# Kernel optimization log

Measured on AMD Instinct MI355X. Metric: run time of the kernel, lower is better.

The kernel has to match this reference:

```python
import jax, jax.numpy as jnp
import numpy as np

N = 8192        # points
M = 131072      # query-key pairs (edges)
C_IN = 512
H = 8           # heads
D = 64          # head_channels
BINS = 48
BIN_SIZE = 0.05


def setup_inputs() -> dict:
    key = jax.random.key(0)
    ks = jax.random.split(key, 8)
    x_F = jax.random.normal(ks[0], (N, C_IN), dtype=jnp.float32)
    x_C = jax.random.uniform(ks[1], (N, 3), dtype=jnp.float32)
    qk_pair_idxs = jax.random.randint(ks[2], (2, M), 0, N, dtype=jnp.int64)
    W_qkv = jax.random.normal(ks[3], (C_IN, 3 * H * D), dtype=jnp.float32) * 0.02
    b_qkv = jnp.zeros((3 * H * D,), dtype=jnp.float32)
    q_tables = jax.random.normal(ks[4], (3, BINS, H, D), dtype=jnp.float32) * 0.02
    k_tables = jax.random.normal(ks[5], (3, BINS, H, D), dtype=jnp.float32) * 0.02
    v_tables = jax.random.normal(ks[6], (3, BINS, H, D), dtype=jnp.float32) * 0.02
    return {"x_F": x_F, "x_C": x_C, "qk_pair_idxs": qk_pair_idxs,
            "W_qkv": W_qkv, "b_qkv": b_qkv,
            "q_tables": q_tables, "k_tables": k_tables, "v_tables": v_tables}


def reference(x_F, x_C, qk_pair_idxs, W_qkv, b_qkv, q_tables, k_tables, v_tables):
    n = x_F.shape[0]
    qkv = (x_F @ W_qkv + b_qkv).reshape(n, 3, H, D)
    q = qkv[:, 0] * (D ** -0.5)   # scale folded into queries, as in the module
    k = qkv[:, 1]
    v = qkv[:, 2]
    qi = qk_pair_idxs[0]
    ki = qk_pair_idxs[1]
    # quantized relative coordinates -> table bin indices [M,3]
    rel = (x_C[qi] - x_C[ki]) / BIN_SIZE + BINS / 2
    idx = jnp.clip(rel.astype(jnp.int32), 0, BINS - 1)
    # precompute per-point, per-axis, per-bin table dot products [N,3,BINS,H]
    q_dot = jnp.einsum('nhd,abhd->nabh', q, q_tables)
    k_dot = jnp.einsum('nhd,abhd->nabh', k, k_tables)
    # content logits [M,H]
    logits = jnp.einsum('mhd,mhd->mh', q[qi], k[ki])
    for a in range(3):  # fixed xyz axes
        logits = logits + q_dot[qi, a, idx[:, a]] + k_dot[ki, a, idx[:, a]]
    # scatter softmax over query index (per head)
    seg_max = jax.ops.segment_max(logits, qi, num_segments=n)
    e = jnp.exp(logits - seg_max[qi])
    denom = jax.ops.segment_sum(e, qi, num_segments=n)
    attn = e / denom[qi]  # [M,H]
    # value-side relative position bias, summed over axes [M,H,D]
    vt = v_tables[0, idx[:, 0]] + v_tables[1, idx[:, 1]] + v_tables[2, idx[:, 2]]
    contrib = attn[:, :, None] * (v[ki] + vt)            # [M,H,D]
    agg = jax.ops.segment_sum(contrib, qi, num_segments=n)  # [N,H,D]
    return agg.reshape(n, H * D)
```

## Files before the change

### kernel.cpp

```cpp
#include <hip/hip_runtime.h>
#include <hip/hip_bf16.h>
#include <stdint.h>

#define N_PTS 8192
#define M_EDGES 131072
#define CIN 512
#define QKV_COLS 1536

typedef __bf16 bf16x8 __attribute__((ext_vector_type(8)));
typedef float f32x4 __attribute__((ext_vector_type(4)));

#define GAS __attribute__((address_space(1)))
#define LAS __attribute__((address_space(3)))

__device__ __forceinline__ void gload_lds16(const void* g, void* l) {
  __builtin_amdgcn_global_load_lds((const GAS void*)g, (LAS void*)l, 16, 0, 0);
}

__global__ __launch_bounds__(256) void prep_kernel(
    const float* __restrict__ xF, const float* __restrict__ W,
    const float* __restrict__ qt, const float* __restrict__ kt,
    const float* __restrict__ vt, const int* __restrict__ pairs,
    const float* __restrict__ xc,
    __bf16* __restrict__ A, __bf16* __restrict__ BT,
    __bf16* __restrict__ qtb, __bf16* __restrict__ ktb, __bf16* __restrict__ vtT,
    int* __restrict__ qi_a, unsigned* __restrict__ pack0, int* __restrict__ cnt) {
  __shared__ float tile[32][33];
  int b = blockIdx.x;
  int tid = threadIdx.x;
  if (b < 4096) {
    int base = (b * 256 + tid) * 4;
    float4 v = *(const float4*)(xF + base);
    A[base + 0] = (__bf16)v.x;
    A[base + 1] = (__bf16)v.y;
    A[base + 2] = (__bf16)v.z;
    A[base + 3] = (__bf16)v.w;
  } else if (b < 4864) {
    int blk = b - 4096;
    int bk = blk & 15, bn = blk >> 4;
    int x = tid & 31, y = tid >> 5;
#pragma unroll
    for (int j = 0; j < 4; j++) {
      int r = y + j * 8;
      tile[r][x] = W[(size_t)(bk * 32 + r) * QKV_COLS + bn * 32 + x];
    }
    __syncthreads();
#pragma unroll
    for (int j = 0; j < 4; j++) {
      int r = y + j * 8;
      BT[(size_t)(bn * 32 + r) * CIN + bk * 32 + x] = (__bf16)tile[x][r];
    }
  } else if (b < 5152) {
    int i = (b - 4864) * 256 + tid;
    int d = i & 63, h = (i >> 6) & 7, ab = i >> 9;
    int po = (h * 144 + ab) * 64 + d;
    qtb[po] = (__bf16)qt[i];
    ktb[po] = (__bf16)kt[i];
  } else if (b < 5472) {
    int i = (b - 5152) * 256 + tid;
    int p = i % 160;
    int d = (i / 160) & 63;
    int h = i / 10240;
    vtT[i] = (p < 144) ? (__bf16)vt[p * 512 + h * 64 + d] : (__bf16)0.f;
  } else {
    int m = (b - 5472) * 256 + tid;
    int qi = pairs[m], ki = pairs[M_EDGES + m];
    unsigned pb = 0;
#pragma unroll
    for (int a = 0; a < 3; a++) {
      float rel = (xc[qi * 3 + a] - xc[ki * 3 + a]) / 0.05f + 24.0f;
      int bb = (int)rel;
      bb = bb < 0 ? 0 : (bb > 47 ? 47 : bb);
      pb |= (unsigned)bb << (6 * a);
    }
    qi_a[m] = qi;
    pack0[m] = (unsigned)ki | (pb << 13);
    atomicAdd(&cnt[qi], 1);
  }
}

__global__ __launch_bounds__(256) void gemm_qkv(const __bf16* __restrict__ A,
                                                const __bf16* __restrict__ BT,
                                                const float* __restrict__ bias,
                                                __bf16* __restrict__ qb,
                                                __bf16* __restrict__ kb,
                                                __bf16* __restrict__ vb) {
  __shared__ __align__(16) char At[64 * 128];
  __shared__ __align__(16) char Bt[128 * 128];
  int tid = threadIdx.x;
  int w = tid >> 6, l = tid & 63;
  int bm = blockIdx.x, bn = blockIdx.y;
  int wm = w & 1, wn = w >> 1;
  f32x4 acc[2][4] = {};
  const char* Ab = (const char*)A;
  const char* Bb = (const char*)BT;
  int lr = l & 15;
  int lk = (l >> 4) * 16;
  int xr = (lr & 7) << 4;

  for (int kt = 0; kt < 8; kt++) {
#pragma unroll
    for (int r = 0; r < 2; r++) {
      int flat = r * 4096 + tid * 16;
      int row = flat >> 7, colb = flat & 127;
      int gcolb = colb ^ ((row & 7) << 4);
      gload_lds16(Ab + ((size_t)(bm * 64 + row) * CIN + kt * 64) * 2 + gcolb,
                  At + r * 4096 + w * 1024);
    }
#pragma unroll
    for (int r = 0; r < 4; r++) {
      int flat = r * 4096 + tid * 16;
      int row = flat >> 7, colb = flat & 127;
      int gcolb = colb ^ ((row & 7) << 4);
      gload_lds16(Bb + ((size_t)(bn * 128 + row) * CIN + kt * 64) * 2 + gcolb,
                  Bt + r * 4096 + w * 1024);
    }
    __syncthreads();
#pragma unroll
    for (int ks = 0; ks < 2; ks++) {
      bf16x8 af[2], bfr[4];
      int cs = (ks * 64 + lk) ^ xr;
#pragma unroll
      for (int mf = 0; mf < 2; mf++) af[mf] = *(const bf16x8*)(At + (wm * 32 + mf * 16 + lr) * 128 + cs);
#pragma unroll
      for (int nf = 0; nf < 4; nf++) bfr[nf] = *(const bf16x8*)(Bt + (wn * 64 + nf * 16 + lr) * 128 + cs);
#pragma unroll
      for (int mf = 0; mf < 2; mf++)
#pragma unroll
        for (int nf = 0; nf < 4; nf++)
          acc[mf][nf] = __builtin_amdgcn_mfma_f32_16x16x32_bf16(af[mf], bfr[nf], acc[mf][nf], 0, 0, 0);
    }
    __syncthreads();
  }

  int lg = l >> 4;
#pragma unroll
  for (int mf = 0; mf < 2; mf++) {
#pragma unroll
    for (int nf = 0; nf < 4; nf++) {
      int gc = bn * 128 + wn * 64 + nf * 16 + lr;
      float b = bias[gc];
      int which = gc >> 9;
      int col = gc & 511;
      __bf16* dst = which == 0 ? qb : (which == 1 ? kb : vb);
      float scale = which == 0 ? 0.125f : 1.0f;
#pragma unroll
      for (int j = 0; j < 4; j++) {
        int gr = bm * 64 + wm * 32 + mf * 16 + lg * 4 + j;
        dst[(size_t)gr * 512 + col] = (__bf16)((acc[mf][nf][j] + b) * scale);
      }
    }
  }
}

__global__ __launch_bounds__(256) void table_dot(const __bf16* __restrict__ qb,
                                                 const __bf16* __restrict__ kb,
                                                 const __bf16* __restrict__ qtb,
                                                 const __bf16* __restrict__ ktb,
                                                 __bf16* __restrict__ qdot,
                                                 __bf16* __restrict__ kdot) {
  __shared__ __align__(16) char As[128 * 128];
  __shared__ __align__(16) char Bs[144 * 128];
  int nt = blockIdx.x, h = blockIdx.y, z = blockIdx.z;
  const __bf16* src = z ? kb : qb;
  const __bf16* tab = z ? ktb : qtb;
  __bf16* out = z ? kdot : qdot;
  int tid = threadIdx.x, w = tid >> 6, l = tid & 63;
  const char* sb = (const char*)src;
  const char* tb = (const char*)tab + (size_t)h * 144 * 128;
#pragma unroll
  for (int p = 0; p < 4; p++) {
    int flat = p * 4096 + tid * 16;
    int row = flat >> 7, colb = flat & 127;
    int gcolb = colb ^ ((row & 7) << 4);
    gload_lds16(sb + (size_t)(nt * 128 + row) * 1024 + h * 128 + gcolb, As + p * 4096 + w * 1024);
    gload_lds16(tb + row * 128 + gcolb, Bs + p * 4096 + w * 1024);
  }
  if (w < 2) {
    int flat = 16384 + w * 1024 + l * 16;
    int row = flat >> 7, colb = flat & 127;
    int gcolb = colb ^ ((row & 7) << 4);
    gload_lds16(tb + row * 128 + gcolb, Bs + 16384 + w * 1024);
  }
  __syncthreads();

  f32x4 acc[2][9] = {};
  int lr = l & 15, lk = (l >> 4) * 16;
  int xr = (lr & 7) << 4;
#pragma unroll
  for (int ks = 0; ks < 2; ks++) {
    bf16x8 af[2], bf[9];
    int cs = (ks * 64 + lk) ^ xr;
#pragma unroll
    for (int mf = 0; mf < 2; mf++)
      af[mf] = *(const bf16x8*)(As + (w * 32 + mf * 16 + lr) * 128 + cs);
#pragma unroll
    for (int nf = 0; nf < 9; nf++)
      bf[nf] = *(const bf16x8*)(Bs + (nf * 16 + lr) * 128 + cs);
#pragma unroll
    for (int mf = 0; mf < 2; mf++)
#pragma unroll
      for (int nf = 0; nf < 9; nf++)
        acc[mf][nf] = __builtin_amdgcn_mfma_f32_16x16x32_bf16(af[mf], bf[nf], acc[mf][nf], 0, 0, 0);
  }

  int lg = l >> 4;
#pragma unroll
  for (int mf = 0; mf < 2; mf++)
#pragma unroll
    for (int nf = 0; nf < 9; nf++)
#pragma unroll
      for (int j = 0; j < 4; j++) {
        int n = nt * 128 + w * 32 + mf * 16 + lg * 4 + j;
        int ab = nf * 16 + lr;
        out[(size_t)n * 1152 + ab * 8 + h] = (__bf16)acc[mf][nf][j];
      }
}

__global__ __launch_bounds__(256) void scan_kernel(const int* __restrict__ cnt,
                                                   int* __restrict__ off,
                                                   int* __restrict__ cursor) {
  __shared__ int wsum[4];
  int tid = threadIdx.x, lane = tid & 63, w = tid >> 6;
  int local[32];
  int s = 0;
#pragma unroll
  for (int i = 0; i < 8; i++) {
    int4 v = ((const int4*)cnt)[tid * 8 + i];
    local[i * 4 + 0] = v.x; local[i * 4 + 1] = v.y;
    local[i * 4 + 2] = v.z; local[i * 4 + 3] = v.w;
    s += v.x + v.y + v.z + v.w;
  }
  int incl = s;
#pragma unroll
  for (int d = 1; d < 64; d <<= 1) {
    int t = __shfl_up(incl, d, 64);
    if (lane >= d) incl += t;
  }
  if (lane == 63) wsum[w] = incl;
  __syncthreads();
  int woff = 0;
#pragma unroll
  for (int j = 0; j < 4; j++) woff += (j < w) ? wsum[j] : 0;
  int run = woff + incl - s;
  int base = tid * 32;
#pragma unroll
  for (int i = 0; i < 32; i++) {
    off[base + i] = run;
    cursor[base + i] = run;
    run += local[i];
  }
  if (tid == 255) off[N_PTS] = run;
}

__global__ void scatter_k(const int* __restrict__ qi_a, const unsigned* __restrict__ pack0,
                          int* __restrict__ cursor, int* __restrict__ qi_s,
                          unsigned* __restrict__ epack) {
  int m = blockIdx.x * blockDim.x + threadIdx.x;
  if (m < M_EDGES) {
    int qi = qi_a[m];
    int pos = atomicAdd(&cursor[qi], 1);
    qi_s[pos] = qi;
    epack[pos] = pack0[m];
  }
}

__global__ void edge_bias(const int* __restrict__ qi_s, const unsigned* __restrict__ epack,
                          const __bf16* __restrict__ qdot, const __bf16* __restrict__ kdot,
                          float* __restrict__ eb) {
  int t = blockIdx.x * 256 + threadIdx.x;
  int e = t >> 3, h = t & 7;
  unsigned pk = epack[e];
  int ki = pk & 8191;
  unsigned pb = pk >> 13;
  int qi = qi_s[e];
  int a0 = ((int)(pb & 63)) * 8 + h;
  int a1 = (48 + (int)((pb >> 6) & 63)) * 8 + h;
  int a2 = (96 + (int)((pb >> 12) & 63)) * 8 + h;
  const __bf16* qd = qdot + qi * 1152;
  const __bf16* kd = kdot + ki * 1152;
  eb[t] = (float)qd[a0] + (float)qd[a1] + (float)qd[a2] +
          (float)kd[a0] + (float)kd[a1] + (float)kd[a2];
}

__global__ __launch_bounds__(512) void attn_kernel(
    const __bf16* __restrict__ qb, const __bf16* __restrict__ kb,
    const __bf16* __restrict__ vb, const float* __restrict__ eb,
    const int* __restrict__ off, const unsigned* __restrict__ epack,
    float* __restrict__ num, float* __restrict__ den, __bf16* __restrict__ Hb) {
  __shared__ float hist[8 * 160];
  int n = blockIdx.x;
  int tid = threadIdx.x;
  int h = tid >> 6, l = tid & 63;
  int es = l >> 3, dg = l & 7;
  int tcol = h * 64 + dg * 8;

  for (int i = tid; i < 1280; i += 512) hist[i] = 0.f;
  __syncthreads();

  bf16x8 q8 = *(const bf16x8*)(qb + (n << 9) + tcol);
  float qv[8];
#pragma unroll
  for (int j = 0; j < 8; j++) qv[j] = (float)q8[j];

  float acc[8] = {0.f, 0.f, 0.f, 0.f, 0.f, 0.f, 0.f, 0.f};
  float dn = 0.f;
  int e0 = off[n], e1 = off[n + 1];

  for (int base = e0; base < e1; base += 8) {
    int e = base + es;
    bool valid = e < e1;
    int ee = valid ? e : e0;
    unsigned pk = epack[ee];
    float ebv = eb[(ee << 3) + h];
    int ki = pk & 8191;
    unsigned pb = pk >> 13;
    bf16x8 k8 = *(const bf16x8*)(kb + (ki << 9) + tcol);
    bf16x8 v8 = *(const bf16x8*)(vb + (ki << 9) + tcol);
    float p = 0.f;
#pragma unroll
    for (int j = 0; j < 8; j++) p += qv[j] * (float)k8[j];
    p += __shfl_xor(p, 1, 64);
    p += __shfl_xor(p, 2, 64);
    p += __shfl_xor(p, 4, 64);
    p += ebv;
    float x = valid ? __expf(p) : 0.f;
    dn += x;
#pragma unroll
    for (int j = 0; j < 8; j++) acc[j] += x * (float)v8[j];
    if (dg == 0 && valid) {
      float* hh = hist + h * 160;
      atomicAdd(hh + (pb & 63), x);
      atomicAdd(hh + 48 + ((pb >> 6) & 63), x);
      atomicAdd(hh + 96 + ((pb >> 12) & 63), x);
    }
  }

#pragma unroll
  for (int s = 8; s <= 32; s <<= 1) {
    dn += __shfl_xor(dn, s, 64);
#pragma unroll
    for (int j = 0; j < 8; j++) acc[j] += __shfl_xor(acc[j], s, 64);
  }

  if (l < 8) {
    float* op = num + (n << 9) + h * 64 + l * 8;
    f32x4 o0 = {acc[0], acc[1], acc[2], acc[3]};
    f32x4 o1 = {acc[4], acc[5], acc[6], acc[7]};
    *(f32x4*)op = o0;
    *(f32x4*)(op + 4) = o1;
  }
  if (l == 0) den[n * 8 + h] = dn;
  __syncthreads();
  for (int i = tid; i < 1280; i += 512) Hb[(size_t)n * 1280 + i] = (__bf16)hist[i];
}

__global__ __launch_bounds__(256) void finish_kernel(const __bf16* __restrict__ Hb,
                                                     const __bf16* __restrict__ vtT,
                                                     const float* __restrict__ den,
                                                     float* __restrict__ out) {
  __shared__ __align__(16) char As[128 * 64];
  __shared__ __align__(16) char Bs[64 * 64];
  int nt = blockIdx.x, h = blockIdx.y;
  int tid = threadIdx.x, w = tid >> 6, l = tid & 63;
  int lr = l & 15, lk = (l >> 4) * 16;
  int xr = (lr & 3) << 4;
  const char* Ab = (const char*)Hb;
  const char* Bb = (const char*)vtT;
  f32x4 acc[2][4] = {};

  for (int kt = 0; kt < 5; kt++) {
#pragma unroll
    for (int c = 0; c < 2; c++) {
      int flat = c * 4096 + tid * 16;
      int row = flat >> 6, colb = flat & 63;
      int gcolb = colb ^ ((row & 3) << 4);
      gload_lds16(Ab + ((size_t)(nt * 128 + row) * 1280 + h * 160 + kt * 32) * 2 + gcolb,
                  As + c * 4096 + w * 1024);
    }
    {
      int flat = tid * 16;
      int row = flat >> 6, colb = flat & 63;
      int gcolb = colb ^ ((row & 3) << 4);
      gload_lds16(Bb + ((size_t)(h * 64 + row) * 160 + kt * 32) * 2 + gcolb,
                  Bs + w * 1024);
    }
    __syncthreads();
    bf16x8 af[2], bf[4];
    int cs = lk ^ xr;
#pragma unroll
    for (int mf = 0; mf < 2; mf++) af[mf] = *(const bf16x8*)(As + (w * 32 + mf * 16 + lr) * 64 + cs);
#pragma unroll
    for (int nf = 0; nf < 4; nf++) bf[nf] = *(const bf16x8*)(Bs + (nf * 16 + lr) * 64 + cs);
#pragma unroll
    for (int mf = 0; mf < 2; mf++)
#pragma unroll
      for (int nf = 0; nf < 4; nf++)
        acc[mf][nf] = __builtin_amdgcn_mfma_f32_16x16x32_bf16(af[mf], bf[nf], acc[mf][nf], 0, 0, 0);
    __syncthreads();
  }

  int lg = l >> 4;
#pragma unroll
  for (int mf = 0; mf < 2; mf++) {
#pragma unroll
    for (int j = 0; j < 4; j++) {
      int n = nt * 128 + w * 32 + mf * 16 + lg * 4 + j;
      float dnv = den[n * 8 + h];
      float inv = dnv > 0.f ? 1.f / dnv : 0.f;
#pragma unroll
      for (int nf = 0; nf < 4; nf++) {
        int gi = (n << 9) + h * 64 + nf * 16 + lr;
        out[gi] = (out[gi] + acc[mf][nf][j]) * inv;
      }
    }
  }
}

extern "C" void kernel_launch(void* const* d_in, const int* in_sizes, int n_in,
                              void* d_out, int out_size, void* d_ws, size_t ws_size,
                              hipStream_t stream) {
  const float* xF = (const float*)d_in[0];
  const float* xC = (const float*)d_in[1];
  const int* pairs = (const int*)d_in[2];
  const float* W = (const float*)d_in[3];
  const float* bias = (const float*)d_in[4];
  const float* qt = (const float*)d_in[5];
  const float* kt = (const float*)d_in[6];
  const float* vt = (const float*)d_in[7];
  float* out = (float*)d_out;

  char* ws = (char*)d_ws;
  size_t o = 0;
  auto alloc = [&](size_t bytes) {
    void* p = ws + o;
    o = (o + bytes + 255) & ~(size_t)255;
    return p;
  };
  char* region0 = (char*)alloc((size_t)N_PTS * 1280 * 2);
  __bf16* A = (__bf16*)region0;
  __bf16* BT = (__bf16*)(region0 + (size_t)N_PTS * CIN * 2);
  __bf16* Hb = (__bf16*)region0;
  __bf16* qb = (__bf16*)alloc((size_t)N_PTS * 512 * 2);
  __bf16* kb = (__bf16*)alloc((size_t)N_PTS * 512 * 2);
  __bf16* vb = (__bf16*)alloc((size_t)N_PTS * 512 * 2);
  __bf16* qtb = (__bf16*)alloc((size_t)8 * 144 * 64 * 2);
  __bf16* ktb = (__bf16*)alloc((size_t)8 * 144 * 64 * 2);
  __bf16* vtT = (__bf16*)alloc((size_t)8 * 64 * 160 * 2);
  __bf16* qdot = (__bf16*)alloc((size_t)N_PTS * 1152 * 2);
  __bf16* kdot = (__bf16*)alloc((size_t)N_PTS * 1152 * 2);
  float* eb = (float*)alloc((size_t)M_EDGES * 8 * 4);
  float* den = (float*)alloc((size_t)N_PTS * 8 * 4);
  int* qi_a = (int*)alloc(M_EDGES * 4);
  unsigned* pack0 = (unsigned*)alloc(M_EDGES * 4);
  int* qi_s = (int*)alloc(M_EDGES * 4);
  unsigned* epack = (unsigned*)alloc(M_EDGES * 4);
  int* cnt = (int*)alloc(N_PTS * 4);
  int* off = (int*)alloc((N_PTS + 1) * 4);
  int* cursor = (int*)alloc(N_PTS * 4);

  hipMemsetAsync(cnt, 0, N_PTS * 4, stream);

  prep_kernel<<<5984, 256, 0, stream>>>(xF, W, qt, kt, vt, pairs, xC,
                                        A, BT, qtb, ktb, vtT, qi_a, pack0, cnt);
  scan_kernel<<<1, 256, 0, stream>>>(cnt, off, cursor);
  scatter_k<<<M_EDGES / 256, 256, 0, stream>>>(qi_a, pack0, cursor, qi_s, epack);
  gemm_qkv<<<dim3(N_PTS / 64, QKV_COLS / 128), 256, 0, stream>>>(A, BT, bias, qb, kb, vb);
  table_dot<<<dim3(N_PTS / 128, 8, 2), 256, 0, stream>>>(qb, kb, qtb, ktb, qdot, kdot);
  edge_bias<<<(M_EDGES * 8) / 256, 256, 0, stream>>>(qi_s, epack, qdot, kdot, eb);
  attn_kernel<<<N_PTS, 512, 0, stream>>>(qb, kb, vb, eb, off, epack, out, den, Hb);
  finish_kernel<<<dim3(N_PTS / 128, 8), 256, 0, stream>>>(Hb, vtT, den, out);
}
```

Measured before the change: 171.9 us.

## Double-buffer GEMM LDS tiles and unroll attention edge loop by two

Adds LDS double buffering to the QKV GEMM and finish GEMM so the next K-tile's global-to-LDS loads are issued before computing on the current tile. The attention kernel now processes two edges per lane per iteration to increase memory-level parallelism for the gathered K/V loads. It also spreads the three histogram atomics across three lanes instead of one. The GEMM grid is transposed so blocks sharing an A row tile run adjacently. Double buffering doubles shared memory use, which may reduce occupancy.

```diff
diff --git a/kernel.cpp b/kernel.cpp
--- a/kernel.cpp
+++ b/kernel.cpp
@@ -85,11 +85,11 @@
                                                 __bf16* __restrict__ qb,
                                                 __bf16* __restrict__ kb,
                                                 __bf16* __restrict__ vb) {
-  __shared__ __align__(16) char At[64 * 128];
-  __shared__ __align__(16) char Bt[128 * 128];
+  __shared__ __align__(16) char At[2][64 * 128];
+  __shared__ __align__(16) char Bt[2][128 * 128];
   int tid = threadIdx.x;
   int w = tid >> 6, l = tid & 63;
-  int bm = blockIdx.x, bn = blockIdx.y;
+  int bn = blockIdx.x, bm = blockIdx.y;
   int wm = w & 1, wn = w >> 1;
   f32x4 acc[2][4] = {};
   const char* Ab = (const char*)A;
@@ -98,32 +98,38 @@
   int lk = (l >> 4) * 16;
   int xr = (lr & 7) << 4;
 
-  for (int kt = 0; kt < 8; kt++) {
+  auto stage = [&](int tk, int buf) {
 #pragma unroll
     for (int r = 0; r < 2; r++) {
       int flat = r * 4096 + tid * 16;
       int row = flat >> 7, colb = flat & 127;
       int gcolb = colb ^ ((row & 7) << 4);
-      gload_lds16(Ab + ((size_t)(bm * 64 + row) * CIN + kt * 64) * 2 + gcolb,
-                  At + r * 4096 + w * 1024);
+      gload_lds16(Ab + ((size_t)(bm * 64 + row) * CIN + tk * 64) * 2 + gcolb,
+                  At[buf] + r * 4096 + w * 1024);
     }
 #pragma unroll
     for (int r = 0; r < 4; r++) {
       int flat = r * 4096 + tid * 16;
       int row = flat >> 7, colb = flat & 127;
       int gcolb = colb ^ ((row & 7) << 4);
-      gload_lds16(Bb + ((size_t)(bn * 128 + row) * CIN + kt * 64) * 2 + gcolb,
-                  Bt + r * 4096 + w * 1024);
-    }
-    __syncthreads();
+      gload_lds16(Bb + ((size_t)(bn * 128 + row) * CIN + tk * 64) * 2 + gcolb,
+                  Bt[buf] + r * 4096 + w * 1024);
+    }
+  };
+
+  stage(0, 0);
+  __syncthreads();
+  int cur = 0;
+  for (int kt = 0; kt < 8; kt++) {
+    if (kt < 7) stage(kt + 1, cur ^ 1);
 #pragma unroll
     for (int ks = 0; ks < 2; ks++) {
       bf16x8 af[2], bfr[4];
       int cs = (ks * 64 + lk) ^ xr;
 #pragma unroll
-      for (int mf = 0; mf < 2; mf++) af[mf] = *(const bf16x8*)(At + (wm * 32 + mf * 16 + lr) * 128 + cs);
-#pragma unroll
-      for (int nf = 0; nf < 4; nf++) bfr[nf] = *(const bf16x8*)(Bt + (wn * 64 + nf * 16 + lr) * 128 + cs);
+      for (int mf = 0; mf < 2; mf++) af[mf] = *(const bf16x8*)(At[cur] + (wm * 32 + mf * 16 + lr) * 128 + cs);
+#pragma unroll
+      for (int nf = 0; nf < 4; nf++) bfr[nf] = *(const bf16x8*)(Bt[cur] + (wn * 64 + nf * 16 + lr) * 128 + cs);
 #pragma unroll
       for (int mf = 0; mf < 2; mf++)
 #pragma unroll
@@ -131,6 +137,7 @@
           acc[mf][nf] = __builtin_amdgcn_mfma_f32_16x16x32_bf16(af[mf], bfr[nf], acc[mf][nf], 0, 0, 0);
     }
     __syncthreads();
+    cur ^= 1;
   }
 
   int lg = l >> 4;
@@ -306,33 +313,46 @@
   float acc[8] = {0.f, 0.f, 0.f, 0.f, 0.f, 0.f, 0.f, 0.f};
   float dn = 0.f;
   int e0 = off[n], e1 = off[n + 1];
-
-  for (int base = e0; base < e1; base += 8) {
-    int e = base + es;
-    bool valid = e < e1;
-    int ee = valid ? e : e0;
-    unsigned pk = epack[ee];
-    float ebv = eb[(ee << 3) + h];
-    int ki = pk & 8191;
-    unsigned pb = pk >> 13;
-    bf16x8 k8 = *(const bf16x8*)(kb + (ki << 9) + tcol);
-    bf16x8 v8 = *(const bf16x8*)(vb + (ki << 9) + tcol);
-    float p = 0.f;
-#pragma unroll
-    for (int j = 0; j < 8; j++) p += qv[j] * (float)k8[j];
-    p += __shfl_xor(p, 1, 64);
-    p += __shfl_xor(p, 2, 64);
-    p += __shfl_xor(p, 4, 64);
-    p += ebv;
-    float x = valid ? __expf(p) : 0.f;
-    dn += x;
-#pragma unroll
-    for (int j = 0; j < 8; j++) acc[j] += x * (float)v8[j];
-    if (dg == 0 && valid) {
-      float* hh = hist + h * 160;
-      atomicAdd(hh + (pb & 63), x);
-      atomicAdd(hh + 48 + ((pb >> 6) & 63), x);
-      atomicAdd(hh + 96 + ((pb >> 12) & 63), x);
+  float* hh = hist + h * 160;
+  int hsh = dg * 6;
+  int hbase = dg * 48;
+
+  for (int base = e0; base < e1; base += 16) {
+    int eA = base + es;
+    int eB = base + 8 + es;
+    int cA = eA < e1 ? eA : e1 - 1;
+    int cB = eB < e1 ? eB : e1 - 1;
+    unsigned pkA = epack[cA], pkB = epack[cB];
+    float ebA = eb[(cA << 3) + h], ebB = eb[(cB << 3) + h];
+    int kiA = pkA & 8191, kiB = pkB & 8191;
+    bf16x8 kA8 = *(const bf16x8*)(kb + (kiA << 9) + tcol);
+    bf16x8 vA8 = *(const bf16x8*)(vb + (kiA << 9) + tcol);
+    bf16x8 kB8 = *(const bf16x8*)(kb + (kiB << 9) + tcol);
+    bf16x8 vB8 = *(const bf16x8*)(vb + (kiB << 9) + tcol);
+    float p1 = 0.f, p2 = 0.f;
+#pragma unroll
+    for (int j = 0; j < 8; j++) {
+      p1 += qv[j] * (float)kA8[j];
+      p2 += qv[j] * (float)kB8[j];
+    }
+    p1 += __shfl_xor(p1, 1, 64);
+    p2 += __shfl_xor(p2, 1, 64);
+    p1 += __shfl_xor(p1, 2, 64);
+    p2 += __shfl_xor(p2, 2, 64);
+    p1 += __shfl_xor(p1, 4, 64);
+    p2 += __shfl_xor(p2, 4, 64);
+    p1 += ebA;
+    p2 += ebB;
+    float x1 = (eA < e1) ? __expf(p1) : 0.f;
+    float x2 = (eB < e1) ? __expf(p2) : 0.f;
+    dn += x1 + x2;
+#pragma unroll
+    for (int j = 0; j < 8; j++)
+      acc[j] += x1 * (float)vA8[j] + x2 * (float)vB8[j];
+    if (dg < 3) {
+      unsigned pbA = pkA >> 13, pbB = pkB >> 13;
+      atomicAdd(hh + hbase + ((pbA >> hsh) & 63), x1);
+      atomicAdd(hh + hbase + ((pbB >> hsh) & 63), x2);
     }
   }
 
@@ -359,8 +379,8 @@
                                                      const __bf16* __restrict__ vtT,
                                                      const float* __restrict__ den,
                                                      float* __restrict__ out) {
-  __shared__ __align__(16) char As[128 * 64];
-  __shared__ __align__(16) char Bs[64 * 64];
+  __shared__ __align__(16) char As[2][128 * 64];
+  __shared__ __align__(16) char Bs[2][64 * 64];
   int nt = blockIdx.x, h = blockIdx.y;
   int tid = threadIdx.x, w = tid >> 6, l = tid & 63;
   int lr = l & 15, lk = (l >> 4) * 16;
@@ -369,35 +389,42 @@
   const char* Bb = (const char*)vtT;
   f32x4 acc[2][4] = {};
 
-  for (int kt = 0; kt < 5; kt++) {
+  auto stage = [&](int tk, int buf) {
 #pragma unroll
     for (int c = 0; c < 2; c++) {
       int flat = c * 4096 + tid * 16;
       int row = flat >> 6, colb = flat & 63;
       int gcolb = colb ^ ((row & 3) << 4);
-      gload_lds16(Ab + ((size_t)(nt * 128 + row) * 1280 + h * 160 + kt * 32) * 2 + gcolb,
-                  As + c * 4096 + w * 1024);
+      gload_lds16(Ab + ((size_t)(nt * 128 + row) * 1280 + h * 160 + tk * 32) * 2 + gcolb,
+                  As[buf] + c * 4096 + w * 1024);
     }
     {
       int flat = tid * 16;
       int row = flat >> 6, colb = flat & 63;
       int gcolb = colb ^ ((row & 3) << 4);
-      gload_lds16(Bb + ((size_t)(h * 64 + row) * 160 + kt * 32) * 2 + gcolb,
-                  Bs + w * 1024);
-    }
-    __syncthreads();
+      gload_lds16(Bb + ((size_t)(h * 64 + row) * 160 + tk * 32) * 2 + gcolb,
+                  Bs[buf] + w * 1024);
+    }
+  };
+
+  stage(0, 0);
+  __syncthreads();
+  int cur = 0;
+  for (int kt = 0; kt < 5; kt++) {
+    if (kt < 4) stage(kt + 1, cur ^ 1);
     bf16x8 af[2], bf[4];
     int cs = lk ^ xr;
 #pragma unroll
-    for (int mf = 0; mf < 2; mf++) af[mf] = *(const bf16x8*)(As + (w * 32 + mf * 16 + lr) * 64 + cs);
-#pragma unroll
-    for (int nf = 0; nf < 4; nf++) bf[nf] = *(const bf16x8*)(Bs + (nf * 16 + lr) * 64 + cs);
+    for (int mf = 0; mf < 2; mf++) af[mf] = *(const bf16x8*)(As[cur] + (w * 32 + mf * 16 + lr) * 64 + cs);
+#pragma unroll
+    for (int nf = 0; nf < 4; nf++) bf[nf] = *(const bf16x8*)(Bs[cur] + (nf * 16 + lr) * 64 + cs);
 #pragma unroll
     for (int mf = 0; mf < 2; mf++)
 #pragma unroll
       for (int nf = 0; nf < 4; nf++)
         acc[mf][nf] = __builtin_amdgcn_mfma_f32_16x16x32_bf16(af[mf], bf[nf], acc[mf][nf], 0, 0, 0);
     __syncthreads();
+    cur ^= 1;
   }
 
   int lg = l >> 4;
@@ -465,7 +492,7 @@
                                         A, BT, qtb, ktb, vtT, qi_a, pack0, cnt);
   scan_kernel<<<1, 256, 0, stream>>>(cnt, off, cursor);
   scatter_k<<<M_EDGES / 256, 256, 0, stream>>>(qi_a, pack0, cursor, qi_s, epack);
-  gemm_qkv<<<dim3(N_PTS / 64, QKV_COLS / 128), 256, 0, stream>>>(A, BT, bias, qb, kb, vb);
+  gemm_qkv<<<dim3(QKV_COLS / 128, N_PTS / 64), 256, 0, stream>>>(A, BT, bias, qb, kb, vb);
   table_dot<<<dim3(N_PTS / 128, 8, 2), 256, 0, stream>>>(qb, kb, qtb, ktb, qdot, kdot);
   edge_bias<<<(M_EDGES * 8) / 256, 256, 0, stream>>>(qi_s, epack, qdot, kdot, eb);
   attn_kernel<<<N_PTS, 512, 0, stream>>>(qb, kb, vb, eb, off, epack, out, den, Hb);
```

Result: slower. 179.9 us (+4.6%).

## Fuse edge bias into attention and double-buffer LDS in GEMM kernels

Applied to the files above, without the earlier changes.

Removes the separate edge_bias kernel and its per-edge fp32 bias buffer. Each attention lane instead gathers one of six qdot/kdot table entries and folds it into the existing shuffle reduction. This also drops the qi_s array from the scatter. Separately, the QKV GEMM and finish GEMM now use double-buffered LDS, so the next k-tile loads while the current one computes. The QKV grid is also transposed so that blocks sharing A rows launch together. This trades extra LDS usage and some lane divergence in the gather for less global traffic and one fewer launch.

```diff
diff --git a/kernel.cpp b/kernel.cpp
--- a/kernel.cpp
+++ b/kernel.cpp
@@ -85,11 +85,11 @@
                                                 __bf16* __restrict__ qb,
                                                 __bf16* __restrict__ kb,
                                                 __bf16* __restrict__ vb) {
-  __shared__ __align__(16) char At[64 * 128];
-  __shared__ __align__(16) char Bt[128 * 128];
+  __shared__ __align__(16) char At[2][64 * 128];
+  __shared__ __align__(16) char Bt[2][128 * 128];
   int tid = threadIdx.x;
   int w = tid >> 6, l = tid & 63;
-  int bm = blockIdx.x, bn = blockIdx.y;
+  int bn = blockIdx.x, bm = blockIdx.y;
   int wm = w & 1, wn = w >> 1;
   f32x4 acc[2][4] = {};
   const char* Ab = (const char*)A;
@@ -98,32 +98,38 @@
   int lk = (l >> 4) * 16;
   int xr = (lr & 7) << 4;
 
-  for (int kt = 0; kt < 8; kt++) {
+  auto stage = [&](int tk, int buf) {
 #pragma unroll
     for (int r = 0; r < 2; r++) {
       int flat = r * 4096 + tid * 16;
       int row = flat >> 7, colb = flat & 127;
       int gcolb = colb ^ ((row & 7) << 4);
-      gload_lds16(Ab + ((size_t)(bm * 64 + row) * CIN + kt * 64) * 2 + gcolb,
-                  At + r * 4096 + w * 1024);
+      gload_lds16(Ab + ((size_t)(bm * 64 + row) * CIN + tk * 64) * 2 + gcolb,
+                  At[buf] + r * 4096 + w * 1024);
     }
 #pragma unroll
     for (int r = 0; r < 4; r++) {
       int flat = r * 4096 + tid * 16;
       int row = flat >> 7, colb = flat & 127;
       int gcolb = colb ^ ((row & 7) << 4);
-      gload_lds16(Bb + ((size_t)(bn * 128 + row) * CIN + kt * 64) * 2 + gcolb,
-                  Bt + r * 4096 + w * 1024);
-    }
-    __syncthreads();
+      gload_lds16(Bb + ((size_t)(bn * 128 + row) * CIN + tk * 64) * 2 + gcolb,
+                  Bt[buf] + r * 4096 + w * 1024);
+    }
+  };
+
+  stage(0, 0);
+  __syncthreads();
+  int cur = 0;
+  for (int kt = 0; kt < 8; kt++) {
+    if (kt < 7) stage(kt + 1, cur ^ 1);
 #pragma unroll
     for (int ks = 0; ks < 2; ks++) {
       bf16x8 af[2], bfr[4];
       int cs = (ks * 64 + lk) ^ xr;
 #pragma unroll
-      for (int mf = 0; mf < 2; mf++) af[mf] = *(const bf16x8*)(At + (wm * 32 + mf * 16 + lr) * 128 + cs);
-#pragma unroll
-      for (int nf = 0; nf < 4; nf++) bfr[nf] = *(const bf16x8*)(Bt + (wn * 64 + nf * 16 + lr) * 128 + cs);
+      for (int mf = 0; mf < 2; mf++) af[mf] = *(const bf16x8*)(At[cur] + (wm * 32 + mf * 16 + lr) * 128 + cs);
+#pragma unroll
+      for (int nf = 0; nf < 4; nf++) bfr[nf] = *(const bf16x8*)(Bt[cur] + (wn * 64 + nf * 16 + lr) * 128 + cs);
 #pragma unroll
       for (int mf = 0; mf < 2; mf++)
 #pragma unroll
@@ -131,6 +137,7 @@
           acc[mf][nf] = __builtin_amdgcn_mfma_f32_16x16x32_bf16(af[mf], bfr[nf], acc[mf][nf], 0, 0, 0);
     }
     __syncthreads();
+    cur ^= 1;
   }
 
   int lg = l >> 4;
@@ -254,39 +261,20 @@
 }
 
 __global__ void scatter_k(const int* __restrict__ qi_a, const unsigned* __restrict__ pack0,
-                          int* __restrict__ cursor, int* __restrict__ qi_s,
-                          unsigned* __restrict__ epack) {
+                          int* __restrict__ cursor, unsigned* __restrict__ epack) {
   int m = blockIdx.x * blockDim.x + threadIdx.x;
   if (m < M_EDGES) {
     int qi = qi_a[m];
     int pos = atomicAdd(&cursor[qi], 1);
-    qi_s[pos] = qi;
     epack[pos] = pack0[m];
   }
-}
-
-__global__ void edge_bias(const int* __restrict__ qi_s, const unsigned* __restrict__ epack,
-                          const __bf16* __restrict__ qdot, const __bf16* __restrict__ kdot,
-                          float* __restrict__ eb) {
-  int t = blockIdx.x * 256 + threadIdx.x;
-  int e = t >> 3, h = t & 7;
-  unsigned pk = epack[e];
-  int ki = pk & 8191;
-  unsigned pb = pk >> 13;
-  int qi = qi_s[e];
-  int a0 = ((int)(pb & 63)) * 8 + h;
-  int a1 = (48 + (int)((pb >> 6) & 63)) * 8 + h;
-  int a2 = (96 + (int)((pb >> 12) & 63)) * 8 + h;
-  const __bf16* qd = qdot + qi * 1152;
-  const __bf16* kd = kdot + ki * 1152;
-  eb[t] = (float)qd[a0] + (float)qd[a1] + (float)qd[a2] +
-          (float)kd[a0] + (float)kd[a1] + (float)kd[a2];
 }
 
 __global__ __launch_bounds__(512) void attn_kernel(
     const __bf16* __restrict__ qb, const __bf16* __restrict__ kb,
-    const __bf16* __restrict__ vb, const float* __restrict__ eb,
-    const int* __restrict__ off, const unsigned* __restrict__ epack,
+    const __bf16* __restrict__ vb, const __bf16* __restrict__ qdot,
+    const __bf16* __restrict__ kdot, const int* __restrict__ off,
+    const unsigned* __restrict__ epack,
     float* __restrict__ num, float* __restrict__ den, __bf16* __restrict__ Hb) {
   __shared__ float hist[8 * 160];
   int n = blockIdx.x;
@@ -306,24 +294,28 @@
   float acc[8] = {0.f, 0.f, 0.f, 0.f, 0.f, 0.f, 0.f, 0.f};
   float dn = 0.f;
   int e0 = off[n], e1 = off[n + 1];
+  const __bf16* qd_row = qdot + (size_t)n * 1152;
+  int axis = dg < 3 ? dg : dg - 3;
+  int tsh = 6 * axis;
 
   for (int base = e0; base < e1; base += 8) {
     int e = base + es;
     bool valid = e < e1;
     int ee = valid ? e : e0;
     unsigned pk = epack[ee];
-    float ebv = eb[(ee << 3) + h];
     int ki = pk & 8191;
     unsigned pb = pk >> 13;
     bf16x8 k8 = *(const bf16x8*)(kb + (ki << 9) + tcol);
     bf16x8 v8 = *(const bf16x8*)(vb + (ki << 9) + tcol);
-    float p = 0.f;
+    int bin = (int)((pb >> tsh) & 63u);
+    int idx = (axis * 48 + bin) * 8 + h;
+    const __bf16* tbl = dg < 3 ? qd_row : (kdot + (size_t)ki * 1152);
+    float p = (dg < 6) ? (float)tbl[idx] : 0.f;
 #pragma unroll
     for (int j = 0; j < 8; j++) p += qv[j] * (float)k8[j];
     p += __shfl_xor(p, 1, 64);
     p += __shfl_xor(p, 2, 64);
     p += __shfl_xor(p, 4, 64);
-    p += ebv;
     float x = valid ? __expf(p) : 0.f;
     dn += x;
 #pragma unroll
@@ -359,8 +351,8 @@
                                                      const __bf16* __restrict__ vtT,
                                                      const float* __restrict__ den,
                                                      float* __restrict__ out) {
-  __shared__ __align__(16) char As[128 * 64];
-  __shared__ __align__(16) char Bs[64 * 64];
+  __shared__ __align__(16) char As[2][128 * 64];
+  __shared__ __align__(16) char Bs[2][64 * 64];
   int nt = blockIdx.x, h = blockIdx.y;
   int tid = threadIdx.x, w = tid >> 6, l = tid & 63;
   int lr = l & 15, lk = (l >> 4) * 16;
@@ -369,35 +361,42 @@
   const char* Bb = (const char*)vtT;
   f32x4 acc[2][4] = {};
 
-  for (int kt = 0; kt < 5; kt++) {
+  auto stage = [&](int tk, int buf) {
 #pragma unroll
     for (int c = 0; c < 2; c++) {
       int flat = c * 4096 + tid * 16;
       int row = flat >> 6, colb = flat & 63;
       int gcolb = colb ^ ((row & 3) << 4);
-      gload_lds16(Ab + ((size_t)(nt * 128 + row) * 1280 + h * 160 + kt * 32) * 2 + gcolb,
-                  As + c * 4096 + w * 1024);
+      gload_lds16(Ab + ((size_t)(nt * 128 + row) * 1280 + h * 160 + tk * 32) * 2 + gcolb,
+                  As[buf] + c * 4096 + w * 1024);
     }
     {
       int flat = tid * 16;
       int row = flat >> 6, colb = flat & 63;
       int gcolb = colb ^ ((row & 3) << 4);
-      gload_lds16(Bb + ((size_t)(h * 64 + row) * 160 + kt * 32) * 2 + gcolb,
-                  Bs + w * 1024);
-    }
-    __syncthreads();
+      gload_lds16(Bb + ((size_t)(h * 64 + row) * 160 + tk * 32) * 2 + gcolb,
+                  Bs[buf] + w * 1024);
+    }
+  };
+
+  stage(0, 0);
+  __syncthreads();
+  int cur = 0;
+  for (int kt = 0; kt < 5; kt++) {
+    if (kt < 4) stage(kt + 1, cur ^ 1);
     bf16x8 af[2], bf[4];
     int cs = lk ^ xr;
 #pragma unroll
-    for (int mf = 0; mf < 2; mf++) af[mf] = *(const bf16x8*)(As + (w * 32 + mf * 16 + lr) * 64 + cs);
-#pragma unroll
-    for (int nf = 0; nf < 4; nf++) bf[nf] = *(const bf16x8*)(Bs + (nf * 16 + lr) * 64 + cs);
+    for (int mf = 0; mf < 2; mf++) af[mf] = *(const bf16x8*)(As[cur] + (w * 32 + mf * 16 + lr) * 64 + cs);
+#pragma unroll
+    for (int nf = 0; nf < 4; nf++) bf[nf] = *(const bf16x8*)(Bs[cur] + (nf * 16 + lr) * 64 + cs);
 #pragma unroll
     for (int mf = 0; mf < 2; mf++)
 #pragma unroll
       for (int nf = 0; nf < 4; nf++)
         acc[mf][nf] = __builtin_amdgcn_mfma_f32_16x16x32_bf16(af[mf], bf[nf], acc[mf][nf], 0, 0, 0);
     __syncthreads();
+    cur ^= 1;
   }
 
   int lg = l >> 4;
@@ -449,11 +448,9 @@
   __bf16* vtT = (__bf16*)alloc((size_t)8 * 64 * 160 * 2);
   __bf16* qdot = (__bf16*)alloc((size_t)N_PTS * 1152 * 2);
   __bf16* kdot = (__bf16*)alloc((size_t)N_PTS * 1152 * 2);
-  float* eb = (float*)alloc((size_t)M_EDGES * 8 * 4);
   float* den = (float*)alloc((size_t)N_PTS * 8 * 4);
   int* qi_a = (int*)alloc(M_EDGES * 4);
   unsigned* pack0 = (unsigned*)alloc(M_EDGES * 4);
-  int* qi_s = (int*)alloc(M_EDGES * 4);
   unsigned* epack = (unsigned*)alloc(M_EDGES * 4);
   int* cnt = (int*)alloc(N_PTS * 4);
   int* off = (int*)alloc((N_PTS + 1) * 4);
@@ -464,10 +461,9 @@
   prep_kernel<<<5984, 256, 0, stream>>>(xF, W, qt, kt, vt, pairs, xC,
                                         A, BT, qtb, ktb, vtT, qi_a, pack0, cnt);
   scan_kernel<<<1, 256, 0, stream>>>(cnt, off, cursor);
-  scatter_k<<<M_EDGES / 256, 256, 0, stream>>>(qi_a, pack0, cursor, qi_s, epack);
-  gemm_qkv<<<dim3(N_PTS / 64, QKV_COLS / 128), 256, 0, stream>>>(A, BT, bias, qb, kb, vb);
+  scatter_k<<<M_EDGES / 256, 256, 0, stream>>>(qi_a, pack0, cursor, epack);
+  gemm_qkv<<<dim3(QKV_COLS / 128, N_PTS / 64), 256, 0, stream>>>(A, BT, bias, qb, kb, vb);
   table_dot<<<dim3(N_PTS / 128, 8, 2), 256, 0, stream>>>(qb, kb, qtb, ktb, qdot, kdot);
-  edge_bias<<<(M_EDGES * 8) / 256, 256, 0, stream>>>(qi_s, epack, qdot, kdot, eb);
-  attn_kernel<<<N_PTS, 512, 0, stream>>>(qb, kb, vb, eb, off, epack, out, den, Hb);
+  attn_kernel<<<N_PTS, 512, 0, stream>>>(qb, kb, vb, qdot, kdot, off, epack, out, den, Hb);
   finish_kernel<<<dim3(N_PTS / 128, 8), 256, 0, stream>>>(Hb, vtT, den, out);
 }
```

Result: faster. 164.9 us (-4.1%).
